# Optimization experiments

Hardware: AMD Instinct MI355X
Metric: run time of the kernel (lower is better)

## Reference

```python
import jax, jax.numpy as jnp
import numpy as np

N_POINTS = 1 << 20
N_LEVELS = 16
F_PER_LVL = 2
LOG2_T = 19
T = 1 << LOG2_T
BASE_RES = 16
PER_LEVEL_SCALE = float(np.exp2(np.log2(2048.0 / 16.0) / (N_LEVELS - 1)))
# 8 trilinear corner offsets [8,3]
OFFSETS = np.stack(np.meshgrid(*([np.array([0, 1])] * 3), indexing='ij'), axis=-1).reshape(8, 3)
PRIMES = np.array([1, 2654435761, 805459861], dtype=np.uint32)  # tcnn spatial hash primes


def _level_params(l):
    # tcnn: grid_scale = 2^(l*log2(s)) * base - 1 ; resolution = ceil(scale)+1
    scale = np.exp2(l * np.log2(PER_LEVEL_SCALE)) * BASE_RES - 1.0
    res = int(np.ceil(scale)) + 1
    return float(scale), res


def hash_encode(x, table):
    """x: [N,3] in [0,1]; table: [L,T,F]. Returns [N, L*F]."""
    offs = jnp.asarray(OFFSETS)                     # [8,3] int32
    primes = jnp.asarray(PRIMES)                    # [3] uint32
    feats = []
    for l in range(N_LEVELS):
        scale, res = _level_params(l)
        pos = x * scale + 0.5                       # [N,3]
        pos_grid = jnp.floor(pos)
        w = pos - pos_grid                          # [N,3] interp weights
        c0 = pos_grid.astype(jnp.int32)             # [N,3]
        corners = c0[None, :, :] + offs[:, None, :]  # [8,N,3]
        if res ** 3 <= T:
            # dense indexing for coarse levels (fits in hashmap)
            cc = jnp.clip(corners, 0, res - 1)
            idx = cc[..., 0] + cc[..., 1] * res + cc[..., 2] * (res * res)
        else:
            cu = corners.astype(jnp.uint32)
            h = (cu[..., 0] * primes[0]) ^ (cu[..., 1] * primes[1]) ^ (cu[..., 2] * primes[2])
            idx = (h & jnp.uint32(T - 1)).astype(jnp.int32)
        f = table[l][idx]                           # [8,N,F] gather
        # trilinear weights: prod over dims of (w if corner bit else 1-w)
        wc = jnp.prod(jnp.where(offs[:, None, :] == 1, w[None], 1.0 - w[None]), axis=-1)  # [8,N]
        feats.append(jnp.sum(wc[..., None] * f, axis=0))  # [N,F]
    return jnp.concatenate(feats, axis=-1)          # [N, 32]


def _softplus10(z):
    return jax.nn.softplus(10.0 * z) / 10.0


def setup_inputs() -> dict:
    key = jax.random.key(0)
    k = jax.random.split(key, 6)
    x = jax.random.uniform(k[0], (N_POINTS, 3), dtype=jnp.float32)
    table = jax.random.normal(k[1], (N_LEVELS, T, F_PER_LVL), dtype=jnp.float32) * 1e-2
    w1 = jax.random.normal(k[2], (64, 32), dtype=jnp.float32) * 0.1
    w2 = jax.random.normal(k[3], (64, 64), dtype=jnp.float32) * 0.1
    w3 = jax.random.normal(k[4], (64, 64), dtype=jnp.float32) * 0.1
    w4 = jax.random.normal(k[5], (1, 64), dtype=jnp.float32) * 0.1
    return {"x": x, "table": table, "w1": w1, "w2": w2, "w3": w3, "w4": w4}


def reference(x, table, w1, w2, w3, w4):
    enc = hash_encode(x, table)                     # [N,32]
    h = _softplus10(enc @ w1.T)
    h = _softplus10(h @ w2.T)
    h = _softplus10(h @ w3.T)
    sdf = h @ w4.T                                  # [N,1]
    return sdf
```

## Files before the change

### kernel.cpp

```cpp
#include <hip/hip_runtime.h>
#include <cmath>

#define T_SIZE (1u << 19)
#define CB 512
#define NBLK 128
#define RCAP 3584

typedef _Float16 h8 __attribute__((ext_vector_type(8)));
typedef _Float16 h4 __attribute__((ext_vector_type(4)));
typedef _Float16 h2 __attribute__((ext_vector_type(2)));
typedef float f4 __attribute__((ext_vector_type(4)));

struct Levels {
    float scale[16];
    int   res[16];
    unsigned dense_mask;
};

__device__ __forceinline__ float softplus10(float z) {
    float e = __builtin_amdgcn_exp2f(fminf(z * 14.426950408889634f, 126.0f));
    return __builtin_amdgcn_logf(1.0f + e) * 0.069314718055994531f;
}

__device__ __forceinline__ unsigned spread3(unsigned v) {
    v &= 1023u;
    v = (v | (v << 16)) & 0x030000FFu;
    v = (v | (v << 8))  & 0x0300F00Fu;
    v = (v | (v << 4))  & 0x030C30C3u;
    v = (v | (v << 2))  & 0x09249249u;
    return v;
}

__device__ __forceinline__ unsigned morton_key(float px, float py, float pz) {
    unsigned qx = (unsigned)fminf(fmaxf(px, 0.f) * 32.f, 31.f);
    unsigned qy = (unsigned)fminf(fmaxf(py, 0.f) * 32.f, 31.f);
    unsigned qz = (unsigned)fminf(fmaxf(pz, 0.f) * 32.f, 31.f);
    return (spread3(qx) << 2) | (spread3(qy) << 1) | spread3(qz);
}

__global__ __launch_bounds__(256) void convert_kernel(
    const float2* __restrict__ t, h2* __restrict__ o, int total4,
    const float* __restrict__ w1, const float* __restrict__ w2,
    const float* __restrict__ w3, _Float16* __restrict__ wh,
    const float* __restrict__ xs, unsigned* __restrict__ M, int N)
{
    const int histStart = (total4 + 10240 + 255) >> 8;
    if ((int)blockIdx.x >= histStart) {
        __shared__ unsigned h[CB];
        const int blk = blockIdx.x - histStart;
        for (int t2 = threadIdx.x; t2 < CB; t2 += 256) h[t2] = 0u;
        __syncthreads();
        const int per = N / NBLK;
        const int s = blk * per;
        for (int i = s + threadIdx.x; i < s + per; i += 256) {
            unsigned k = morton_key(xs[3 * i], xs[3 * i + 1], xs[3 * i + 2]) >> 6;
            atomicAdd(&h[k], 1u);
        }
        __syncthreads();
        for (int t2 = threadIdx.x; t2 < CB; t2 += 256)
            M[t2 * NBLK + blk] = h[t2];
        return;
    }
    int i = blockIdx.x * 256 + threadIdx.x;
    if (i < total4) {
        const float2* src = t + (size_t)i * 4;
        h8 r;
#pragma unroll
        for (int j = 0; j < 4; ++j) {
            float2 v = src[j];
            r[2 * j]     = (_Float16)v.x;
            r[2 * j + 1] = (_Float16)v.y;
        }
        *(h8*)(o + (size_t)i * 4) = r;
    } else {
        int k = i - total4;
        if (k < 10240) {
            float v = (k < 2048) ? w1[k] : (k < 6144) ? w2[k - 2048] : w3[k - 6144];
            wh[k] = (_Float16)v;
        }
    }
}

__global__ __launch_bounds__(1024) void scan_kernel(
    const unsigned* __restrict__ M, unsigned* __restrict__ Ms)
{
    __shared__ unsigned tmp[1024];
    const int t = threadIdx.x;
    const int PER = (CB * NBLK) / 1024;
    unsigned s = 0;
    for (int j = 0; j < PER; ++j) s += M[t * PER + j];
    tmp[t] = s;
    __syncthreads();
    for (int d = 1; d < 1024; d <<= 1) {
        unsigned v = (t >= d) ? tmp[t - d] : 0u;
        __syncthreads();
        tmp[t] += v;
        __syncthreads();
    }
    unsigned run = (t > 0) ? tmp[t - 1] : 0u;
    for (int j = 0; j < PER; ++j) {
        unsigned v = M[t * PER + j];
        Ms[t * PER + j] = run;
        run += v;
    }
}

__global__ __launch_bounds__(256) void cscatter_kernel(
    const float* __restrict__ xs, const unsigned* __restrict__ Ms,
    float4* __restrict__ sx4, int N)
{
    __shared__ unsigned cur[CB];
    for (int t = threadIdx.x; t < CB; t += 256)
        cur[t] = Ms[t * NBLK + blockIdx.x];
    __syncthreads();
    const int per = N / NBLK;
    const int s = blockIdx.x * per;
    for (int i = s + threadIdx.x; i < s + per; i += 256) {
        float px = xs[3 * i], py = xs[3 * i + 1], pz = xs[3 * i + 2];
        unsigned k = morton_key(px, py, pz) >> 6;
        unsigned pos = atomicAdd(&cur[k], 1u);
        sx4[pos] = make_float4(px, py, pz, __uint_as_float((unsigned)i));
    }
}

__global__ __launch_bounds__(256) void refine_kernel(
    float4* __restrict__ sx4, const unsigned* __restrict__ Ms, int N)
{
    __shared__ float4 pts[RCAP];
    __shared__ unsigned h[64], base[64];
    const int b = blockIdx.x;
    const unsigned s = Ms[b * NBLK];
    const unsigned e = (b == CB - 1) ? (unsigned)N : Ms[(b + 1) * NBLK];
    const unsigned cnt = e - s;
    if (cnt > RCAP) return;
    if (threadIdx.x < 64) h[threadIdx.x] = 0u;
    __syncthreads();
    for (unsigned i = threadIdx.x; i < cnt; i += 256) {
        float4 q = sx4[s + i];
        pts[i] = q;
        unsigned k = morton_key(q.x, q.y, q.z) & 63u;
        atomicAdd(&h[k], 1u);
    }
    __syncthreads();
    if (threadIdx.x == 0) {
        unsigned a = 0;
        for (int j = 0; j < 64; ++j) { base[j] = a; a += h[j]; }
    }
    __syncthreads();
    if (threadIdx.x < 64) h[threadIdx.x] = 0u;
    __syncthreads();
    for (unsigned i = threadIdx.x; i < cnt; i += 256) {
        float4 q = pts[i];
        unsigned k = morton_key(q.x, q.y, q.z) & 63u;
        unsigned r = base[k] + atomicAdd(&h[k], 1u);
        sx4[s + r] = q;
    }
}

__device__ __forceinline__ void gather_pair(
    const h2* __restrict__ tl, unsigned i0, unsigned i1,
    float2& v0, float2& v1)
{
    unsigned g = i0 & ~3u;
    union { h8 v; uint4 u; } cv;
    cv.v = *(const h8*)(tl + g);
    unsigned p0 = i0 & 3u;
    unsigned a01 = (p0 & 1u) ? cv.u.y : cv.u.x;
    unsigned a23 = (p0 & 1u) ? cv.u.w : cv.u.z;
    unsigned e0  = (p0 & 2u) ? a23 : a01;
    unsigned e1;
    if ((i1 & ~3u) == g) {
        unsigned p1 = i1 & 3u;
        unsigned b01 = (p1 & 1u) ? cv.u.y : cv.u.x;
        unsigned b23 = (p1 & 1u) ? cv.u.w : cv.u.z;
        e1 = (p1 & 2u) ? b23 : b01;
    } else {
        e1 = *(const unsigned*)(tl + i1);
    }
    h2 c0 = __builtin_bit_cast(h2, e0);
    h2 c1 = __builtin_bit_cast(h2, e1);
    v0 = make_float2((float)c0[0], (float)c0[1]);
    v1 = make_float2((float)c1[0], (float)c1[1]);
}

__device__ __forceinline__ h2 encode_point(
    float px, float py, float pz, float s, int res, bool dense,
    const h2* __restrict__ tl)
{
    float fx = px * s + 0.5f, fy = py * s + 0.5f, fz = pz * s + 0.5f;
    float gx = floorf(fx), gy = floorf(fy), gz = floorf(fz);
    float wx = fx - gx, wy = fy - gy, wz = fz - gz;
    int cx = (int)gx, cy = (int)gy, cz = (int)gz;

    float2 vx0[4], vx1[4];
    if (dense) {
        int r1 = res - 1;
        int x0 = min(cx, r1), x1 = min(cx + 1, r1);
        int y0 = min(cy, r1), y1 = min(cy + 1, r1);
        int z0 = min(cz, r1), z1 = min(cz + 1, r1);
        int rr = res * res;
        int bases[4] = {y0 * res + z0 * rr, y0 * res + z1 * rr,
                        y1 * res + z0 * rr, y1 * res + z1 * rr};
#pragma unroll
        for (int j = 0; j < 4; ++j)
            gather_pair(tl, (unsigned)(x0 + bases[j]), (unsigned)(x1 + bases[j]),
                        vx0[j], vx1[j]);
    } else {
        unsigned hy0 = (unsigned)cy * 2654435761u, hy1 = (unsigned)(cy + 1) * 2654435761u;
        unsigned hz0 = (unsigned)cz * 805459861u,  hz1 = (unsigned)(cz + 1) * 805459861u;
        unsigned Y[4] = {hy0 ^ hz0, hy0 ^ hz1, hy1 ^ hz0, hy1 ^ hz1};
        const unsigned M = T_SIZE - 1;
#pragma unroll
        for (int j = 0; j < 4; ++j)
            gather_pair(tl, ((unsigned)cx ^ Y[j]) & M,
                        ((unsigned)(cx + 1) ^ Y[j]) & M, vx0[j], vx1[j]);
    }

    float wx0 = 1.f - wx, wy0 = 1.f - wy, wz0 = 1.f - wz;
    float wyz[4] = {wy0 * wz0, wy0 * wz, wy * wz0, wy * wz};
    float f0 = 0.f, f1 = 0.f;
#pragma unroll
    for (int j = 0; j < 4; ++j) {
        float w0 = wx0 * wyz[j], w1 = wx * wyz[j];
        f0 += w0 * vx0[j].x + w1 * vx1[j].x;
        f1 += w0 * vx0[j].y + w1 * vx1[j].y;
    }
    h2 r; r[0] = (_Float16)f0; r[1] = (_Float16)f1;
    return r;
}

template <bool SORTED>
__global__ __launch_bounds__(256, 3) void fused_all_kernel(
    const float* __restrict__ xs, const float4* __restrict__ xs4,
    const h2* __restrict__ table16,
    const _Float16* __restrict__ w1, const _Float16* __restrict__ w2,
    const _Float16* __restrict__ w3, const float* __restrict__ w4,
    float* __restrict__ out, Levels lv, int N)
{
    constexpr int AR = 72;
    __shared__ __align__(16) char smem[4 * 9216];
    __shared__ float sx[768];

    const int tid  = threadIdx.x;
    const int wave = tid >> 6;
    const int lane = tid & 63;
    const int lrow = lane & 15;
    const int quad = lane >> 4;
    const int base = blockIdx.x * 256;
    char* wmem = smem + wave * 9216;
    const f4 zero = {0.f, 0.f, 0.f, 0.f};

    float px, py, pz;
    unsigned oi = 0;
    if constexpr (SORTED) {
        float4 q = xs4[base + tid];
        px = q.x; py = q.y; pz = q.z;
        oi = __float_as_uint(q.w);
    } else {
        for (int t = tid; t < 768; t += 256) sx[t] = xs[(size_t)base * 3 + t];
        __syncthreads();
        px = sx[tid * 3]; py = sx[tid * 3 + 1]; pz = sx[tid * 3 + 2];
    }
    const int p = tid & 63;

    const int GORD[4] = {3, 2, 1, 0};
#pragma unroll
    for (int gi = 0; gi < 4; ++gi) {
        const int g = GORD[gi];
        h8 pack;
#pragma unroll
        for (int s4 = 0; s4 < 4; ++s4) {
            const int l = g * 4 + ((g == 3) ? ((s4 + 3) & 3) : s4);
            h2 v = encode_point(px, py, pz, lv.scale[l], lv.res[l],
                                (lv.dense_mask >> l) & 1u,
                                table16 + (size_t)l * T_SIZE);
            pack[2 * (l & 3)]     = v[0];
            pack[2 * (l & 3) + 1] = v[1];
        }
        *(h8*)(wmem + (g << 10) + (p << 4)) = pack;
    }

    asm volatile("" ::: "memory");

    h8 aW1[4];
#pragma unroll
    for (int tm = 0; tm < 4; ++tm)
        aW1[tm] = *(const h8*)(w1 + (tm * 16 + lrow) * 32 + quad * 8);
    h8 aW2[4][2], aW3[4][2];
#pragma unroll
    for (int tm = 0; tm < 4; ++tm)
#pragma unroll
        for (int km = 0; km < 2; ++km) {
            aW2[tm][km] = *(const h8*)(w2 + (tm * 16 + lrow) * 64 + km * 32 + quad * 8);
            aW3[tm][km] = *(const h8*)(w3 + (tm * 16 + lrow) * 64 + km * 32 + quad * 8);
        }
    h4 w4q[4];
#pragma unroll
    for (int tm = 0; tm < 4; ++tm)
#pragma unroll
        for (int r = 0; r < 4; ++r) w4q[tm][r] = (_Float16)w4[tm * 16 + quad * 4 + r];

    h8 bin[4];
#pragma unroll
    for (int t = 0; t < 4; ++t)
        bin[t] = *(const h8*)(wmem + (quad << 10) + ((t * 16 + lrow) << 4));

    _Float16* wAct = (_Float16*)wmem;

#pragma unroll
    for (int t = 0; t < 4; ++t) {
        const int arow = (t * 16 + lrow) * AR;
#pragma unroll
        for (int tm = 0; tm < 4; ++tm) {
            f4 acc = __builtin_amdgcn_mfma_f32_16x16x32_f16(aW1[tm], bin[t], zero, 0, 0, 0);
            h4 pk;
#pragma unroll
            for (int r = 0; r < 4; ++r) pk[r] = (_Float16)softplus10(acc[r]);
            *(h4*)&wAct[arow + tm * 16 + quad * 4] = pk;
        }
    }

#pragma unroll
    for (int t = 0; t < 4; ++t) {
        const int arow = (t * 16 + lrow) * AR;
        h8 b0 = *(const h8*)&wAct[arow + quad * 8];
        h8 b1 = *(const h8*)&wAct[arow + 32 + quad * 8];
        f4 accs[4];
#pragma unroll
        for (int tm = 0; tm < 4; ++tm) {
            f4 acc = __builtin_amdgcn_mfma_f32_16x16x32_f16(aW2[tm][0], b0, zero, 0, 0, 0);
            acc     = __builtin_amdgcn_mfma_f32_16x16x32_f16(aW2[tm][1], b1, acc,  0, 0, 0);
            accs[tm] = acc;
        }
#pragma unroll
        for (int tm = 0; tm < 4; ++tm) {
            h4 pk;
#pragma unroll
            for (int r = 0; r < 4; ++r) pk[r] = (_Float16)softplus10(accs[tm][r]);
            *(h4*)&wAct[arow + tm * 16 + quad * 4] = pk;
        }
    }

#pragma unroll
    for (int t = 0; t < 4; ++t) {
        const int arow = (t * 16 + lrow) * AR;
        h8 b0 = *(const h8*)&wAct[arow + quad * 8];
        h8 b1 = *(const h8*)&wAct[arow + 32 + quad * 8];
        float sum = 0.f;
#pragma unroll
        for (int tm = 0; tm < 4; ++tm) {
            f4 acc = __builtin_amdgcn_mfma_f32_16x16x32_f16(aW3[tm][0], b0, zero, 0, 0, 0);
            acc     = __builtin_amdgcn_mfma_f32_16x16x32_f16(aW3[tm][1], b1, acc,  0, 0, 0);
#pragma unroll
            for (int r = 0; r < 4; ++r)
                sum += (float)w4q[tm][r] * softplus10(acc[r]);
        }
        sum += __shfl_xor(sum, 16, 64);
        sum += __shfl_xor(sum, 32, 64);
        if constexpr (SORTED) {
            unsigned t_oi = __shfl(oi, t * 16 + lrow, 64);
            if (quad == 0) out[t_oi] = sum;
        } else {
            if (quad == 0)
                out[base + wave * 64 + t * 16 + lrow] = sum;
        }
    }
}

__global__ __launch_bounds__(256) void encode_kernel_f32(
    const float* __restrict__ xs, const float2* __restrict__ table,
    h2* __restrict__ enc2, Levels lv, int N)
{
    const int i = blockIdx.x * 256 + threadIdx.x;
    const int l = blockIdx.y;
    if (i >= N) return;
    float px = xs[3 * i], py = xs[3 * i + 1], pz = xs[3 * i + 2];
    float s = lv.scale[l];
    int res = lv.res[l];
    float fx = px * s + 0.5f, fy = py * s + 0.5f, fz = pz * s + 0.5f;
    float gx = floorf(fx), gy = floorf(fy), gz = floorf(fz);
    float wx = fx - gx, wy = fy - gy, wz = fz - gz;
    int cx = (int)gx, cy = (int)gy, cz = (int)gz;
    unsigned idx[8];
    if ((lv.dense_mask >> l) & 1u) {
        int r1 = res - 1;
        int x0 = min(cx, r1), x1 = min(cx + 1, r1);
        int y0 = min(cy, r1), y1 = min(cy + 1, r1);
        int z0 = min(cz, r1), z1 = min(cz + 1, r1);
        int rr = res * res;
        idx[0] = x0 + y0 * res + z0 * rr; idx[1] = x0 + y0 * res + z1 * rr;
        idx[2] = x0 + y1 * res + z0 * rr; idx[3] = x0 + y1 * res + z1 * rr;
        idx[4] = x1 + y0 * res + z0 * rr; idx[5] = x1 + y0 * res + z1 * rr;
        idx[6] = x1 + y1 * res + z0 * rr; idx[7] = x1 + y1 * res + z1 * rr;
    } else {
        unsigned hx0 = (unsigned)cx, hx1 = (unsigned)(cx + 1);
        unsigned hy0 = (unsigned)cy * 2654435761u, hy1 = (unsigned)(cy + 1) * 2654435761u;
        unsigned hz0 = (unsigned)cz * 805459861u,  hz1 = (unsigned)(cz + 1) * 805459861u;
        idx[0] = (hx0^hy0^hz0) & (T_SIZE-1); idx[1] = (hx0^hy0^hz1) & (T_SIZE-1);
        idx[2] = (hx0^hy1^hz0) & (T_SIZE-1); idx[3] = (hx0^hy1^hz1) & (T_SIZE-1);
        idx[4] = (hx1^hy0^hz0) & (T_SIZE-1); idx[5] = (hx1^hy0^hz1) & (T_SIZE-1);
        idx[6] = (hx1^hy1^hz0) & (T_SIZE-1); idx[7] = (hx1^hy1^hz1) & (T_SIZE-1);
    }
    const float2* tl = table + (size_t)l * T_SIZE;
    float wx0 = 1.f - wx, wy0 = 1.f - wy, wz0 = 1.f - wz;
    float wcs[8] = {wx0*wy0*wz0, wx0*wy0*wz, wx0*wy*wz0, wx0*wy*wz,
                    wx*wy0*wz0,  wx*wy0*wz,  wx*wy*wz0,  wx*wy*wz};
    float f0 = 0.f, f1 = 0.f;
#pragma unroll
    for (int c = 0; c < 8; ++c) {
        float2 v = tl[idx[c]];
        f0 += wcs[c] * v.x; f1 += wcs[c] * v.y;
    }
    h2 r; r[0] = (_Float16)f0; r[1] = (_Float16)f1;
    enc2[(size_t)l * N + i] = r;
}

__global__ __launch_bounds__(256, 3) void fused_staged_f32(
    const h2* __restrict__ enc2,
    const float* __restrict__ w1, const float* __restrict__ w2,
    const float* __restrict__ w3, const float* __restrict__ w4,
    float* __restrict__ out, int N)
{
    constexpr int AR = 72;
    __shared__ __align__(16) char smem[4 * 9216];
    const int tid  = threadIdx.x;
    const int wave = tid >> 6;
    const int lane = tid & 63;
    const int lrow = lane & 15;
    const int quad = lane >> 4;
    const int base = blockIdx.x * 256;
    char* wmem = smem + wave * 9216;
    const f4 zero = {0.f, 0.f, 0.f, 0.f};
    const int p = tid & 63;
#pragma unroll
    for (int l = 0; l < 16; ++l) {
        h2 v = enc2[(size_t)l * N + base + tid];
        *(h2*)(wmem + ((l >> 2) << 10) + (p << 4) + ((l & 3) << 2)) = v;
    }
    asm volatile("" ::: "memory");
    h8 aW1[4];
#pragma unroll
    for (int tm = 0; tm < 4; ++tm) {
        h8 r;
#pragma unroll
        for (int j = 0; j < 8; ++j)
            r[j] = (_Float16)w1[(tm * 16 + lrow) * 32 + quad * 8 + j];
        aW1[tm] = r;
    }
    h8 aW2[4][2], aW3[4][2];
#pragma unroll
    for (int tm = 0; tm < 4; ++tm)
#pragma unroll
        for (int km = 0; km < 2; ++km) {
            h8 r2, r3;
#pragma unroll
            for (int j = 0; j < 8; ++j) {
                r2[j] = (_Float16)w2[(tm * 16 + lrow) * 64 + km * 32 + quad * 8 + j];
                r3[j] = (_Float16)w3[(tm * 16 + lrow) * 64 + km * 32 + quad * 8 + j];
            }
            aW2[tm][km] = r2; aW3[tm][km] = r3;
        }
    h4 w4q[4];
#pragma unroll
    for (int tm = 0; tm < 4; ++tm)
#pragma unroll
        for (int r = 0; r < 4; ++r) w4q[tm][r] = (_Float16)w4[tm * 16 + quad * 4 + r];
    h8 bin[4];
#pragma unroll
    for (int t = 0; t < 4; ++t)
        bin[t] = *(const h8*)(wmem + (quad << 10) + ((t * 16 + lrow) << 4));
    _Float16* wAct = (_Float16*)wmem;
#pragma unroll
    for (int t = 0; t < 4; ++t) {
        const int arow = (t * 16 + lrow) * AR;
#pragma unroll
        for (int tm = 0; tm < 4; ++tm) {
            f4 acc = __builtin_amdgcn_mfma_f32_16x16x32_f16(aW1[tm], bin[t], zero, 0, 0, 0);
            h4 pk;
#pragma unroll
            for (int r = 0; r < 4; ++r) pk[r] = (_Float16)softplus10(acc[r]);
            *(h4*)&wAct[arow + tm * 16 + quad * 4] = pk;
        }
    }
#pragma unroll
    for (int t = 0; t < 4; ++t) {
        const int arow = (t * 16 + lrow) * AR;
        h8 b0 = *(const h8*)&wAct[arow + quad * 8];
        h8 b1 = *(const h8*)&wAct[arow + 32 + quad * 8];
        f4 accs[4];
#pragma unroll
        for (int tm = 0; tm < 4; ++tm) {
            f4 acc = __builtin_amdgcn_mfma_f32_16x16x32_f16(aW2[tm][0], b0, zero, 0, 0, 0);
            acc     = __builtin_amdgcn_mfma_f32_16x16x32_f16(aW2[tm][1], b1, acc,  0, 0, 0);
            accs[tm] = acc;
        }
#pragma unroll
        for (int tm = 0; tm < 4; ++tm) {
            h4 pk;
#pragma unroll
            for (int r = 0; r < 4; ++r) pk[r] = (_Float16)softplus10(accs[tm][r]);
            *(h4*)&wAct[arow + tm * 16 + quad * 4] = pk;
        }
    }
#pragma unroll
    for (int t = 0; t < 4; ++t) {
        const int arow = (t * 16 + lrow) * AR;
        h8 b0 = *(const h8*)&wAct[arow + quad * 8];
        h8 b1 = *(const h8*)&wAct[arow + 32 + quad * 8];
        float sum = 0.f;
#pragma unroll
        for (int tm = 0; tm < 4; ++tm) {
            f4 acc = __builtin_amdgcn_mfma_f32_16x16x32_f16(aW3[tm][0], b0, zero, 0, 0, 0);
            acc     = __builtin_amdgcn_mfma_f32_16x16x32_f16(aW3[tm][1], b1, acc,  0, 0, 0);
#pragma unroll
            for (int r = 0; r < 4; ++r)
                sum += (float)w4q[tm][r] * softplus10(acc[r]);
        }
        sum += __shfl_xor(sum, 16, 64);
        sum += __shfl_xor(sum, 32, 64);
        if (quad == 0)
            out[base + wave * 64 + t * 16 + lrow] = sum;
    }
}

extern "C" void kernel_launch(void* const* d_in, const int* in_sizes, int n_in,
                              void* d_out, int out_size, void* d_ws, size_t ws_size,
                              hipStream_t stream) {
    const float* x     = (const float*)d_in[0];
    const float* table = (const float*)d_in[1];
    const float* w1    = (const float*)d_in[2];
    const float* w2    = (const float*)d_in[3];
    const float* w3    = (const float*)d_in[4];
    const float* w4    = (const float*)d_in[5];
    float* out = (float*)d_out;
    const int N = in_sizes[0] / 3;

    Levels lv;
    lv.dense_mask = 0;
    const double pls = exp2(log2(2048.0 / 16.0) / 15.0);
    const double lg  = log2(pls);
    for (int l = 0; l < 16; ++l) {
        double sc = exp2((double)l * lg) * 16.0 - 1.0;
        int res = (int)ceil(sc) + 1;
        lv.scale[l] = (float)sc;
        lv.res[l]   = res;
        if ((long long)res * res * res <= (long long)T_SIZE) lv.dense_mask |= (1u << l);
    }

    const size_t tableBytes = (size_t)16 * T_SIZE * 4;
    const size_t whBytes    = 32768;
    const size_t sx4Bytes   = (size_t)N * 16;
    const size_t mBytes     = (size_t)CB * NBLK * 4;

    const int ptBlocks = (N + 255) / 256;
    const int total4 = 16 * T_SIZE / 4;
    const int convBlocks = (total4 + 10240 + 255) / 256;

    if (ws_size >= tableBytes + whBytes + sx4Bytes + 2 * mBytes
        && N == NBLK * 8192) {
        h2* table16    = (h2*)d_ws;
        _Float16* wh   = (_Float16*)((char*)d_ws + tableBytes);
        float4* sx4    = (float4*)((char*)d_ws + tableBytes + whBytes);
        unsigned* M    = (unsigned*)((char*)d_ws + tableBytes + whBytes + sx4Bytes);
        unsigned* Ms   = M + (size_t)CB * NBLK;

        hipLaunchKernelGGL(convert_kernel, dim3(convBlocks + NBLK), dim3(256), 0,
                           stream, (const float2*)table, table16, total4,
                           w1, w2, w3, wh, x, M, N);
        hipLaunchKernelGGL(scan_kernel, dim3(1), dim3(1024), 0, stream, M, Ms);
        hipLaunchKernelGGL(cscatter_kernel, dim3(NBLK), dim3(256), 0, stream,
                           x, Ms, sx4, N);
        hipLaunchKernelGGL(refine_kernel, dim3(CB), dim3(256), 0, stream,
                           sx4, Ms, N);

        hipLaunchKernelGGL((fused_all_kernel<true>), dim3(ptBlocks), dim3(256),
                           0, stream, x, (const float4*)sx4, (const h2*)table16,
                           wh, wh + 2048, wh + 6144, w4, out, lv, N);
    } else if (ws_size >= tableBytes + whBytes) {
        h2* table16 = (h2*)d_ws;
        _Float16* wh = (_Float16*)((char*)d_ws + tableBytes);
        hipLaunchKernelGGL(convert_kernel, dim3(convBlocks), dim3(256), 0, stream,
                           (const float2*)table, table16, total4, w1, w2, w3, wh,
                           x, (unsigned*)nullptr, N);
        hipLaunchKernelGGL((fused_all_kernel<false>), dim3(ptBlocks), dim3(256),
                           0, stream, x, (const float4*)nullptr, (const h2*)table16,
                           wh, wh + 2048, wh + 6144, w4, out, lv, N);
    } else {
        h2* enc2 = (h2*)d_ws;
        hipLaunchKernelGGL(encode_kernel_f32, dim3(ptBlocks, 16), dim3(256), 0, stream,
                           x, (const float2*)table, enc2, lv, N);
        hipLaunchKernelGGL(fused_staged_f32, dim3(ptBlocks), dim3(256),
                           0, stream, (const h2*)enc2, w1, w2, w3, w4, out, N);
    }
}
```

Before: 519.7 us.

## Overlap fine-level hash encoding with Morton sort stages in combined kernels

The hash-encoding of the five finest levels (10-14) moves out of the fused MLP kernel. It now runs in extra blocks appended to the scan, scatter and refine sort kernels, so those gathers overlap with the low-parallelism sorting work and are written to an unsorted per-point buffer. The fused kernel then reads those five features by original index and computes only the remaining 11 levels on sorted points. The refine step now reads from global memory and writes to a second buffer, with no shared-memory staging or capacity bailout. This costs extra workspace, an extra 32 B/point write and read, and the fine levels are gathered in unsorted order, which loses the cache locality the Morton sort provided.

```diff
diff --git a/kernel.cpp b/kernel.cpp
--- a/kernel.cpp
+++ b/kernel.cpp
@@ -4,7 +4,6 @@
 #define T_SIZE (1u << 19)
 #define CB 512
 #define NBLK 128
-#define RCAP 3584
 
 typedef _Float16 h8 __attribute__((ext_vector_type(8)));
 typedef _Float16 h4 __attribute__((ext_vector_type(4)));
@@ -78,82 +77,6 @@
             float v = (k < 2048) ? w1[k] : (k < 6144) ? w2[k - 2048] : w3[k - 6144];
             wh[k] = (_Float16)v;
         }
-    }
-}
-
-__global__ __launch_bounds__(1024) void scan_kernel(
-    const unsigned* __restrict__ M, unsigned* __restrict__ Ms)
-{
-    __shared__ unsigned tmp[1024];
-    const int t = threadIdx.x;
-    const int PER = (CB * NBLK) / 1024;
-    unsigned s = 0;
-    for (int j = 0; j < PER; ++j) s += M[t * PER + j];
-    tmp[t] = s;
-    __syncthreads();
-    for (int d = 1; d < 1024; d <<= 1) {
-        unsigned v = (t >= d) ? tmp[t - d] : 0u;
-        __syncthreads();
-        tmp[t] += v;
-        __syncthreads();
-    }
-    unsigned run = (t > 0) ? tmp[t - 1] : 0u;
-    for (int j = 0; j < PER; ++j) {
-        unsigned v = M[t * PER + j];
-        Ms[t * PER + j] = run;
-        run += v;
-    }
-}
-
-__global__ __launch_bounds__(256) void cscatter_kernel(
-    const float* __restrict__ xs, const unsigned* __restrict__ Ms,
-    float4* __restrict__ sx4, int N)
-{
-    __shared__ unsigned cur[CB];
-    for (int t = threadIdx.x; t < CB; t += 256)
-        cur[t] = Ms[t * NBLK + blockIdx.x];
-    __syncthreads();
-    const int per = N / NBLK;
-    const int s = blockIdx.x * per;
-    for (int i = s + threadIdx.x; i < s + per; i += 256) {
-        float px = xs[3 * i], py = xs[3 * i + 1], pz = xs[3 * i + 2];
-        unsigned k = morton_key(px, py, pz) >> 6;
-        unsigned pos = atomicAdd(&cur[k], 1u);
-        sx4[pos] = make_float4(px, py, pz, __uint_as_float((unsigned)i));
-    }
-}
-
-__global__ __launch_bounds__(256) void refine_kernel(
-    float4* __restrict__ sx4, const unsigned* __restrict__ Ms, int N)
-{
-    __shared__ float4 pts[RCAP];
-    __shared__ unsigned h[64], base[64];
-    const int b = blockIdx.x;
-    const unsigned s = Ms[b * NBLK];
-    const unsigned e = (b == CB - 1) ? (unsigned)N : Ms[(b + 1) * NBLK];
-    const unsigned cnt = e - s;
-    if (cnt > RCAP) return;
-    if (threadIdx.x < 64) h[threadIdx.x] = 0u;
-    __syncthreads();
-    for (unsigned i = threadIdx.x; i < cnt; i += 256) {
-        float4 q = sx4[s + i];
-        pts[i] = q;
-        unsigned k = morton_key(q.x, q.y, q.z) & 63u;
-        atomicAdd(&h[k], 1u);
-    }
-    __syncthreads();
-    if (threadIdx.x == 0) {
-        unsigned a = 0;
-        for (int j = 0; j < 64; ++j) { base[j] = a; a += h[j]; }
-    }
-    __syncthreads();
-    if (threadIdx.x < 64) h[threadIdx.x] = 0u;
-    __syncthreads();
-    for (unsigned i = threadIdx.x; i < cnt; i += 256) {
-        float4 q = pts[i];
-        unsigned k = morton_key(q.x, q.y, q.z) & 63u;
-        unsigned r = base[k] + atomicAdd(&h[k], 1u);
-        sx4[s + r] = q;
     }
 }
 
@@ -229,17 +152,128 @@
     return r;
 }
 
-template <bool SORTED>
-__global__ __launch_bounds__(256, 3) void fused_all_kernel(
-    const float* __restrict__ xs, const float4* __restrict__ xs4,
-    const h2* __restrict__ table16,
+__device__ __forceinline__ void encode_block_body(
+    const float* __restrict__ xs, const h2* __restrict__ table16,
+    h2* __restrict__ enc5, const Levels& lv, int l, int blk,
+    unsigned* shbuf)
+{
+    float* sx = (float*)shbuf;
+    const int i0 = blk * 256;
+    for (int t = threadIdx.x; t < 768; t += 256) sx[t] = xs[(size_t)i0 * 3 + t];
+    __syncthreads();
+    const int i = i0 + threadIdx.x;
+    h2 r = encode_point(sx[threadIdx.x * 3], sx[threadIdx.x * 3 + 1],
+                        sx[threadIdx.x * 3 + 2], lv.scale[l], lv.res[l],
+                        (lv.dense_mask >> l) & 1u, table16 + (size_t)l * T_SIZE);
+    enc5[(size_t)i * 8 + (l - 10)] = r;
+}
+
+__global__ __launch_bounds__(256) void k2_scan_enc(
+    const unsigned* __restrict__ M, unsigned* __restrict__ Ms,
+    const float* __restrict__ xs, const h2* __restrict__ table16,
+    h2* __restrict__ enc5, Levels lv, int N)
+{
+    __shared__ unsigned shbuf[768];
+    if (blockIdx.x == 0) {
+        unsigned* tmp = shbuf;
+        const int t = threadIdx.x;
+        unsigned s = 0;
+        for (int j = 0; j < 256; ++j) s += M[t * 256 + j];
+        tmp[t] = s;
+        __syncthreads();
+        for (int d = 1; d < 256; d <<= 1) {
+            unsigned v = (t >= d) ? tmp[t - d] : 0u;
+            __syncthreads();
+            tmp[t] += v;
+            __syncthreads();
+        }
+        unsigned run = (t > 0) ? tmp[t - 1] : 0u;
+        for (int j = 0; j < 256; ++j) {
+            unsigned v = M[t * 256 + j];
+            Ms[t * 256 + j] = run;
+            run += v;
+        }
+        return;
+    }
+    encode_block_body(xs, table16, enc5, lv, 14, blockIdx.x - 1, shbuf);
+}
+
+__global__ __launch_bounds__(256) void k3_csc_enc(
+    const float* __restrict__ xs, const unsigned* __restrict__ Ms,
+    float4* __restrict__ sx4a, const h2* __restrict__ table16,
+    h2* __restrict__ enc5, Levels lv, int N)
+{
+    __shared__ unsigned shbuf[768];
+    if ((int)blockIdx.x < NBLK) {
+        unsigned* cur = shbuf;
+        for (int t = threadIdx.x; t < CB; t += 256)
+            cur[t] = Ms[t * NBLK + blockIdx.x];
+        __syncthreads();
+        const int per = N / NBLK;
+        const int s = blockIdx.x * per;
+        for (int i = s + threadIdx.x; i < s + per; i += 256) {
+            float px = xs[3 * i], py = xs[3 * i + 1], pz = xs[3 * i + 2];
+            unsigned k = morton_key(px, py, pz) >> 6;
+            unsigned pos = atomicAdd(&cur[k], 1u);
+            sx4a[pos] = make_float4(px, py, pz, __uint_as_float((unsigned)i));
+        }
+        return;
+    }
+    int r = blockIdx.x - NBLK;
+    int l = (r < 4096) ? 13 : 12;
+    encode_block_body(xs, table16, enc5, lv, l, r & 4095, shbuf);
+}
+
+__global__ __launch_bounds__(256) void k4_ref_enc(
+    const float* __restrict__ xs, const unsigned* __restrict__ Ms,
+    const float4* __restrict__ sx4a, float4* __restrict__ sx4b,
+    const h2* __restrict__ table16, h2* __restrict__ enc5, Levels lv, int N)
+{
+    __shared__ unsigned shbuf[768];
+    if ((int)blockIdx.x < CB) {
+        unsigned* h  = shbuf;
+        unsigned* bs = shbuf + 64;
+        const int b = blockIdx.x;
+        const unsigned s = Ms[b * NBLK];
+        const unsigned e = (b == CB - 1) ? (unsigned)N : Ms[(b + 1) * NBLK];
+        const unsigned cnt = e - s;
+        if (threadIdx.x < 64) h[threadIdx.x] = 0u;
+        __syncthreads();
+        for (unsigned i = threadIdx.x; i < cnt; i += 256) {
+            float4 q = sx4a[s + i];
+            unsigned k = morton_key(q.x, q.y, q.z) & 63u;
+            atomicAdd(&h[k], 1u);
+        }
+        __syncthreads();
+        if (threadIdx.x == 0) {
+            unsigned a = 0;
+            for (int j = 0; j < 64; ++j) { bs[j] = a; a += h[j]; }
+        }
+        __syncthreads();
+        if (threadIdx.x < 64) h[threadIdx.x] = 0u;
+        __syncthreads();
+        for (unsigned i = threadIdx.x; i < cnt; i += 256) {
+            float4 q = sx4a[s + i];
+            unsigned k = morton_key(q.x, q.y, q.z) & 63u;
+            unsigned r2 = atomicAdd(&h[k], 1u);
+            sx4b[s + bs[k] + r2] = q;
+        }
+        return;
+    }
+    int r = blockIdx.x - CB;
+    int l = (r < 4096) ? 11 : 10;
+    encode_block_body(xs, table16, enc5, lv, l, r & 4095, shbuf);
+}
+
+__global__ __launch_bounds__(256, 3) void fused_kernel(
+    const float4* __restrict__ xs4, const h2* __restrict__ table16,
+    const h2* __restrict__ enc5,
     const _Float16* __restrict__ w1, const _Float16* __restrict__ w2,
     const _Float16* __restrict__ w3, const float* __restrict__ w4,
     float* __restrict__ out, Levels lv, int N)
 {
     constexpr int AR = 72;
     __shared__ __align__(16) char smem[4 * 9216];
-    __shared__ float sx[768];
 
     const int tid  = threadIdx.x;
     const int wave = tid >> 6;
@@ -250,35 +284,27 @@
     char* wmem = smem + wave * 9216;
     const f4 zero = {0.f, 0.f, 0.f, 0.f};
 
-    float px, py, pz;
-    unsigned oi = 0;
-    if constexpr (SORTED) {
-        float4 q = xs4[base + tid];
-        px = q.x; py = q.y; pz = q.z;
-        oi = __float_as_uint(q.w);
-    } else {
-        for (int t = tid; t < 768; t += 256) sx[t] = xs[(size_t)base * 3 + t];
-        __syncthreads();
-        px = sx[tid * 3]; py = sx[tid * 3 + 1]; pz = sx[tid * 3 + 2];
-    }
+    float4 q = xs4[base + tid];
+    const float px = q.x, py = q.y, pz = q.z;
+    const unsigned oi = __float_as_uint(q.w);
     const int p = tid & 63;
 
-    const int GORD[4] = {3, 2, 1, 0};
-#pragma unroll
-    for (int gi = 0; gi < 4; ++gi) {
-        const int g = GORD[gi];
-        h8 pack;
-#pragma unroll
-        for (int s4 = 0; s4 < 4; ++s4) {
-            const int l = g * 4 + ((g == 3) ? ((s4 + 3) & 3) : s4);
-            h2 v = encode_point(px, py, pz, lv.scale[l], lv.res[l],
-                                (lv.dense_mask >> l) & 1u,
-                                table16 + (size_t)l * T_SIZE);
-            pack[2 * (l & 3)]     = v[0];
-            pack[2 * (l & 3) + 1] = v[1];
-        }
-        *(h8*)(wmem + (g << 10) + (p << 4)) = pack;
-    }
+    union { uint4 u[2]; h2 h[8]; } s8;
+    s8.u[0] = *(const uint4*)(enc5 + (size_t)oi * 8);
+    s8.u[1] = *(const uint4*)(enc5 + (size_t)oi * 8 + 4);
+
+    const int LMAP[11] = {15, 5, 6, 7, 8, 9, 0, 1, 2, 3, 4};
+#pragma unroll
+    for (int s6 = 0; s6 < 11; ++s6) {
+        const int l = LMAP[s6];
+        h2 v = encode_point(px, py, pz, lv.scale[l], lv.res[l],
+                            (lv.dense_mask >> l) & 1u,
+                            table16 + (size_t)l * T_SIZE);
+        *(h2*)(wmem + ((l >> 2) << 10) + (p << 4) + ((l & 3) << 2)) = v;
+    }
+#pragma unroll
+    for (int l = 10; l < 15; ++l)
+        *(h2*)(wmem + ((l >> 2) << 10) + (p << 4) + ((l & 3) << 2)) = s8.h[l - 10];
 
     asm volatile("" ::: "memory");
 
@@ -357,13 +383,111 @@
         }
         sum += __shfl_xor(sum, 16, 64);
         sum += __shfl_xor(sum, 32, 64);
-        if constexpr (SORTED) {
-            unsigned t_oi = __shfl(oi, t * 16 + lrow, 64);
-            if (quad == 0) out[t_oi] = sum;
-        } else {
-            if (quad == 0)
-                out[base + wave * 64 + t * 16 + lrow] = sum;
-        }
+        unsigned t_oi = __shfl(oi, t * 16 + lrow, 64);
+        if (quad == 0) out[t_oi] = sum;
+    }
+}
+
+__global__ __launch_bounds__(256, 3) void fused_all_kernel(
+    const float* __restrict__ xs, const h2* __restrict__ table16,
+    const _Float16* __restrict__ w1, const _Float16* __restrict__ w2,
+    const _Float16* __restrict__ w3, const float* __restrict__ w4,
+    float* __restrict__ out, Levels lv, int N)
+{
+    constexpr int AR = 72;
+    __shared__ __align__(16) char smem[4 * 9216];
+    __shared__ float sx[768];
+    const int tid  = threadIdx.x;
+    const int wave = tid >> 6;
+    const int lane = tid & 63;
+    const int lrow = lane & 15;
+    const int quad = lane >> 4;
+    const int base = blockIdx.x * 256;
+    char* wmem = smem + wave * 9216;
+    const f4 zero = {0.f, 0.f, 0.f, 0.f};
+    for (int t = tid; t < 768; t += 256) sx[t] = xs[(size_t)base * 3 + t];
+    __syncthreads();
+    const float px = sx[tid * 3], py = sx[tid * 3 + 1], pz = sx[tid * 3 + 2];
+    const int p = tid & 63;
+#pragma unroll
+    for (int l = 0; l < 16; ++l) {
+        h2 v = encode_point(px, py, pz, lv.scale[l], lv.res[l],
+                            (lv.dense_mask >> l) & 1u, table16 + (size_t)l * T_SIZE);
+        *(h2*)(wmem + ((l >> 2) << 10) + (p << 4) + ((l & 3) << 2)) = v;
+    }
+    asm volatile("" ::: "memory");
+    h8 aW1[4];
+#pragma unroll
+    for (int tm = 0; tm < 4; ++tm)
+        aW1[tm] = *(const h8*)(w1 + (tm * 16 + lrow) * 32 + quad * 8);
+    h8 aW2[4][2], aW3[4][2];
+#pragma unroll
+    for (int tm = 0; tm < 4; ++tm)
+#pragma unroll
+        for (int km = 0; km < 2; ++km) {
+            aW2[tm][km] = *(const h8*)(w2 + (tm * 16 + lrow) * 64 + km * 32 + quad * 8);
+            aW3[tm][km] = *(const h8*)(w3 + (tm * 16 + lrow) * 64 + km * 32 + quad * 8);
+        }
+    h4 w4q[4];
+#pragma unroll
+    for (int tm = 0; tm < 4; ++tm)
+#pragma unroll
+        for (int r = 0; r < 4; ++r) w4q[tm][r] = (_Float16)w4[tm * 16 + quad * 4 + r];
+    h8 bin[4];
+#pragma unroll
+    for (int t = 0; t < 4; ++t)
+        bin[t] = *(const h8*)(wmem + (quad << 10) + ((t * 16 + lrow) << 4));
+    _Float16* wAct = (_Float16*)wmem;
+#pragma unroll
+    for (int t = 0; t < 4; ++t) {
+        const int arow = (t * 16 + lrow) * AR;
+#pragma unroll
+        for (int tm = 0; tm < 4; ++tm) {
+            f4 acc = __builtin_amdgcn_mfma_f32_16x16x32_f16(aW1[tm], bin[t], zero, 0, 0, 0);
+            h4 pk;
+#pragma unroll
+            for (int r = 0; r < 4; ++r) pk[r] = (_Float16)softplus10(acc[r]);
+            *(h4*)&wAct[arow + tm * 16 + quad * 4] = pk;
+        }
+    }
+#pragma unroll
+    for (int t = 0; t < 4; ++t) {
+        const int arow = (t * 16 + lrow) * AR;
+        h8 b0 = *(const h8*)&wAct[arow + quad * 8];
+        h8 b1 = *(const h8*)&wAct[arow + 32 + quad * 8];
+        f4 accs[4];
+#pragma unroll
+        for (int tm = 0; tm < 4; ++tm) {
+            f4 acc = __builtin_amdgcn_mfma_f32_16x16x32_f16(aW2[tm][0], b0, zero, 0, 0, 0);
+            acc     = __builtin_amdgcn_mfma_f32_16x16x32_f16(aW2[tm][1], b1, acc,  0, 0, 0);
+            accs[tm] = acc;
+        }
+#pragma unroll
+        for (int tm = 0; tm < 4; ++tm) {
+            h4 pk;
+#pragma unroll
+            for (int r = 0; r < 4; ++r) pk[r] = (_Float16)softplus10(accs[tm][r]);
+            *(h4*)&wAct[arow + tm * 16 + quad * 4] = pk;
+        }
+    }
+#pragma unroll
+    for (int t = 0; t < 4; ++t) {
+        const int arow = (t * 16 + lrow) * AR;
+        h8 b0 = *(const h8*)&wAct[arow + quad * 8];
+        h8 b1 = *(const h8*)&wAct[arow + 32 + quad * 8];
+        float sum = 0.f;
+#pragma unroll
+        for (int tm = 0; tm < 4; ++tm) {
+            f4 acc = __builtin_amdgcn_mfma_f32_16x16x32_f16(aW3[tm][0], b0, zero, 0, 0, 0);
+            acc     = __builtin_amdgcn_mfma_f32_16x16x32_f16(aW3[tm][1], b1, acc,  0, 0, 0);
+#pragma unroll
+            for (int r = 0; r < 4; ++r)
+                sum += (float)w4q[tm][r] * softplus10(acc[r]);
+        }
+        sum += __shfl_xor(sum, 16, 64);
+        sum += __shfl_xor(sum, 32, 64);
+        if (quad == 0)
+            out[base + wave * 64 + t * 16 + lrow] = sum;
     }
 }
 
@@ -549,32 +673,37 @@
 
     const size_t tableBytes = (size_t)16 * T_SIZE * 4;
     const size_t whBytes    = 32768;
-    const size_t sx4Bytes   = (size_t)N * 16;
+    const size_t sxBytes    = (size_t)N * 16;
     const size_t mBytes     = (size_t)CB * NBLK * 4;
+    const size_t encBytes   = (size_t)N * 32;
 
     const int ptBlocks = (N + 255) / 256;
     const int total4 = 16 * T_SIZE / 4;
     const int convBlocks = (total4 + 10240 + 255) / 256;
 
-    if (ws_size >= tableBytes + whBytes + sx4Bytes + 2 * mBytes
+    if (ws_size >= tableBytes + whBytes + 2 * sxBytes + 2 * mBytes + encBytes
         && N == NBLK * 8192) {
-        h2* table16    = (h2*)d_ws;
-        _Float16* wh   = (_Float16*)((char*)d_ws + tableBytes);
-        float4* sx4    = (float4*)((char*)d_ws + tableBytes + whBytes);
-        unsigned* M    = (unsigned*)((char*)d_ws + tableBytes + whBytes + sx4Bytes);
-        unsigned* Ms   = M + (size_t)CB * NBLK;
+        char* wsb = (char*)d_ws;
+        h2* table16    = (h2*)wsb;                        wsb += tableBytes;
+        _Float16* wh   = (_Float16*)wsb;                  wsb += whBytes;
+        float4* sx4a   = (float4*)wsb;                    wsb += sxBytes;
+        float4* sx4b   = (float4*)wsb;                    wsb += sxBytes;
+        unsigned* M    = (unsigned*)wsb;                  wsb += mBytes;
+        unsigned* Ms   = (unsigned*)wsb;                  wsb += mBytes;
+        h2* enc5       = (h2*)wsb;
 
         hipLaunchKernelGGL(convert_kernel, dim3(convBlocks + NBLK), dim3(256), 0,
                            stream, (const float2*)table, table16, total4,
                            w1, w2, w3, wh, x, M, N);
-        hipLaunchKernelGGL(scan_kernel, dim3(1), dim3(1024), 0, stream, M, Ms);
-        hipLaunchKernelGGL(cscatter_kernel, dim3(NBLK), dim3(256), 0, stream,
-                           x, Ms, sx4, N);
-        hipLaunchKernelGGL(refine_kernel, dim3(CB), dim3(256), 0, stream,
-                           sx4, Ms, N);
-
-        hipLaunchKernelGGL((fused_all_kernel<true>), dim3(ptBlocks), dim3(256),
-                           0, stream, x, (const float4*)sx4, (const h2*)table16,
+        hipLaunchKernelGGL(k2_scan_enc, dim3(1 + ptBlocks), dim3(256), 0, stream,
+                           M, Ms, x, (const h2*)table16, enc5, lv, N);
+        hipLaunchKernelGGL(k3_csc_enc, dim3(NBLK + 2 * ptBlocks), dim3(256), 0,
+                           stream, x, Ms, sx4a, (const h2*)table16, enc5, lv, N);
+        hipLaunchKernelGGL(k4_ref_enc, dim3(CB + 2 * ptBlocks), dim3(256), 0,
+                           stream, x, Ms, (const float4*)sx4a, sx4b,
+                           (const h2*)table16, enc5, lv, N);
+        hipLaunchKernelGGL(fused_kernel, dim3(ptBlocks), dim3(256), 0, stream,
+                           (const float4*)sx4b, (const h2*)table16, (const h2*)enc5,
                            wh, wh + 2048, wh + 6144, w4, out, lv, N);
     } else if (ws_size >= tableBytes + whBytes) {
         h2* table16 = (h2*)d_ws;
@@ -582,8 +711,8 @@
         hipLaunchKernelGGL(convert_kernel, dim3(convBlocks), dim3(256), 0, stream,
                            (const float2*)table, table16, total4, w1, w2, w3, wh,
                            x, (unsigned*)nullptr, N);
-        hipLaunchKernelGGL((fused_all_kernel<false>), dim3(ptBlocks), dim3(256),
-                           0, stream, x, (const float4*)nullptr, (const h2*)table16,
+        hipLaunchKernelGGL(fused_all_kernel, dim3(ptBlocks), dim3(256),
+                           0, stream, x, (const h2*)table16,
                            wh, wh + 2048, wh + 6144, w4, out, lv, N);
     } else {
         h2* enc2 = (h2*)d_ws;
```

Result: faster. 456.0 us (-12.3%).
